# Optimization experiments

Hardware: AMD Instinct MI355X
Metric: run time of the kernel (lower is better)

The kernel has to match this reference:

```python
import jax, jax.numpy as jnp
import numpy as np

N_HEAD = 16
N_EMBD = 1024


def setup_inputs() -> dict:
    key = jax.random.key(0)
    k1, k2 = jax.random.split(key)
    x = jax.random.normal(k1, (2, 2048, N_EMBD), dtype=jnp.float32)
    # nn.Linear(n_embd, 3*n_embd, bias=False); store as [in, out] for x @ w
    w_qkv = jax.random.normal(k2, (N_EMBD, 3 * N_EMBD), dtype=jnp.float32) * (N_EMBD ** -0.5)
    return {"x": x, "w_qkv": w_qkv}


def reference(x, w_qkv):
    B, T, C = x.shape
    H = N_HEAD
    D = C // H  # head dim
    qkv = x @ w_qkv  # [B, T, 3C]
    q, k, v = jnp.split(qkv, 3, axis=2)
    # [B, T, H, D] -> [B, H, T, D]
    q = q.reshape(B, T, H, D).transpose(0, 2, 1, 3)
    k = k.reshape(B, T, H, D).transpose(0, 2, 1, 3)
    v = v.reshape(B, T, H, D).transpose(0, 2, 1, 3)
    att = jnp.einsum('bhtd,bhsd->bhts', q, k) / np.sqrt(D).astype(np.float32)
    causal = jnp.tril(jnp.ones((T, T), dtype=bool))  # [T, T]
    att = jnp.where(causal, att, -jnp.inf)
    att = jax.nn.softmax(att, axis=-1)
    out = jnp.einsum('bhts,bhsd->bhtd', att, v)  # [B, H, T, D]
    return out.transpose(0, 2, 1, 3).reshape(B, T, C)
```

## Files before the change

kernel.cpp:

```cpp
#include <hip/hip_runtime.h>
#include <hip/hip_bf16.h>

#define BATCH 2
#define SEQ   2048
#define EMBD  1024
#define NHEAD 16
#define HDIM  64
#define N3    3072
#define MTOT  4096
#define KDIM  1024

typedef __attribute__((ext_vector_type(8))) short  short8;
typedef __attribute__((ext_vector_type(4))) short  s16x4;
typedef __attribute__((ext_vector_type(4))) unsigned short u16x4;
typedef __attribute__((ext_vector_type(4))) float  f32x4;

__device__ __forceinline__ unsigned short f2bf(float f) {
    unsigned int u = __builtin_bit_cast(unsigned int, f);
    u += 0x7fffu + ((u >> 16) & 1u);
    return (unsigned short)(u >> 16);
}

__global__ __launch_bounds__(256) void cast_x_kernel(const float* __restrict__ x,
                                                     short* __restrict__ xb, int n4) {
    int i = blockIdx.x * 256 + threadIdx.x;
    if (i >= n4) return;
    float4 f = reinterpret_cast<const float4*>(x)[i];
    s16x4 o;
    o[0] = (short)f2bf(f.x); o[1] = (short)f2bf(f.y);
    o[2] = (short)f2bf(f.z); o[3] = (short)f2bf(f.w);
    reinterpret_cast<s16x4*>(xb)[i] = o;
}

__global__ __launch_bounds__(256) void cast_wt_kernel(const float* __restrict__ w,
                                                      short* __restrict__ wt) {
    __shared__ float tile[32][33];
    int n0 = blockIdx.x * 32;
    int k0 = blockIdx.y * 32;
    int tx = threadIdx.x & 31;
    int ty = threadIdx.x >> 5;
#pragma unroll
    for (int i = 0; i < 4; ++i)
        tile[ty + i * 8][tx] = w[(size_t)(k0 + ty + i * 8) * N3 + n0 + tx];
    __syncthreads();
#pragma unroll
    for (int i = 0; i < 4; ++i)
        wt[(size_t)(n0 + ty + i * 8) * KDIM + k0 + tx] = (short)f2bf(tile[tx][ty + i * 8]);
}

__device__ __forceinline__ void stage_tile(const short* gbase, short* lbase, int tid) {
#pragma unroll
    for (int c = 0; c < 2; ++c) {
        int row = c * 64 + (tid >> 2);
        int chunk = tid & 3;
        const short* gp = gbase + (size_t)row * KDIM + chunk * 8;
        short* lp = lbase + c * 2048 + tid * 8;
        __builtin_amdgcn_global_load_lds((const __attribute__((address_space(1))) void*)gp,
                                         (__attribute__((address_space(3))) void*)lp,
                                         16, 0, 0);
    }
}

__global__ __launch_bounds__(256) void qkv_gemm_kernel(const short* __restrict__ xb,
                                                       const short* __restrict__ wt,
                                                       short* __restrict__ qb,
                                                       short* __restrict__ kbuf,
                                                       short* __restrict__ vt) {
    __shared__ short lA[2][128 * 32];
    __shared__ short lB[2][128 * 32];

    const int tid  = threadIdx.x;
    const int lane = tid & 63;
    const int wid  = tid >> 6;
    const int wm = wid >> 1, wn = wid & 1;
    const int m0 = blockIdx.y * 128;
    const int n0 = blockIdx.x * 128;

    f32x4 acc[4][4];
#pragma unroll
    for (int i = 0; i < 4; ++i)
#pragma unroll
        for (int j = 0; j < 4; ++j) acc[i][j] = (f32x4){0.f, 0.f, 0.f, 0.f};

    const short* gA = xb + (size_t)m0 * KDIM;
    const short* gB = wt + (size_t)n0 * KDIM;

    stage_tile(gA, lA[0], tid);
    stage_tile(gB, lB[0], tid);
    asm volatile("s_waitcnt vmcnt(0)" ::: "memory");
    __syncthreads();

    int cur = 0;
    const int arow = (lane & 15) * 32 + (lane >> 4) * 8;
#pragma unroll 1
    for (int kt = 0; kt < KDIM / 32; ++kt) {
        if (kt + 1 < KDIM / 32) {
            stage_tile(gA + (kt + 1) * 32, lA[cur ^ 1], tid);
            stage_tile(gB + (kt + 1) * 32, lB[cur ^ 1], tid);
        }
        short8 a[4], b[4];
#pragma unroll
        for (int im = 0; im < 4; ++im)
            a[im] = *(const short8*)&lA[cur][(wm * 64 + im * 16) * 32 + arow];
#pragma unroll
        for (int in = 0; in < 4; ++in)
            b[in] = *(const short8*)&lB[cur][(wn * 64 + in * 16) * 32 + arow];
#pragma unroll
        for (int im = 0; im < 4; ++im)
#pragma unroll
            for (int in = 0; in < 4; ++in)
                acc[im][in] = __builtin_amdgcn_mfma_f32_16x16x32_bf16(a[im], b[in], acc[im][in], 0, 0, 0);
        asm volatile("s_waitcnt vmcnt(0)" ::: "memory");
        __syncthreads();
        cur ^= 1;
    }

#pragma unroll
    for (int im = 0; im < 4; ++im) {
        int t0m = m0 + wm * 64 + im * 16 + (lane >> 4) * 4;
        int b = t0m >> 11;
        int t0 = t0m & 2047;
#pragma unroll
        for (int in = 0; in < 4; ++in) {
            int col = n0 + wn * 64 + in * 16 + (lane & 15);
            int which = col >> 10;
            int h = (col >> 6) & 15;
            int d = col & 63;
            if (which == 2) {
                u16x4 pk;
#pragma unroll
                for (int r = 0; r < 4; ++r) pk[r] = f2bf(acc[im][in][r]);
                *(u16x4*)&vt[((size_t)(b * NHEAD + h) * HDIM + d) * SEQ + t0] = pk;
            } else {
                short* dst = (which == 0) ? qb : kbuf;
#pragma unroll
                for (int r = 0; r < 4; ++r)
                    dst[((size_t)(b * NHEAD + h) * SEQ + t0 + r) * HDIM + d] = (short)f2bf(acc[im][in][r]);
            }
        }
    }
}

#define KVB 64

__device__ __forceinline__ int swzf(int r) { return (r & 3) ^ (((r >> 2) & 3) << 1); }

__device__ __forceinline__ void stage_kv(const short* kh, const short* vh, int kb,
                                         short* lk, short* lv, int tid) {
#pragma unroll
    for (int c = 0; c < 2; ++c) {
        int row = c * 32 + (tid >> 3);
        int sch = (tid & 7) ^ swzf(row);
        const short* gk = kh + (size_t)(kb + row) * HDIM + sch * 8;
        short* lpk = lk + c * 2048 + tid * 8;
        __builtin_amdgcn_global_load_lds((const __attribute__((address_space(1))) void*)gk,
                                         (__attribute__((address_space(3))) void*)lpk, 16, 0, 0);
        const short* gv = vh + (size_t)row * SEQ + kb + sch * 8;
        short* lpv = lv + c * 2048 + tid * 8;
        __builtin_amdgcn_global_load_lds((const __attribute__((address_space(1))) void*)gv,
                                         (__attribute__((address_space(3))) void*)lpv, 16, 0, 0);
    }
}

__global__ __launch_bounds__(256) void attn_kernel(const short* __restrict__ q,
                                                   const short* __restrict__ kk,
                                                   const short* __restrict__ vtg,
                                                   float* __restrict__ out) {
    const int tid  = threadIdx.x;
    const int lane = tid & 63;
    const int wid  = tid >> 6;
    const int pid = blockIdx.x;
    const int bh = blockIdx.y;
    const int rbase = lane & 15;
    const int hi    = lane >> 4;

    const short* qh = q   + (size_t)bh * SEQ * HDIM;
    const short* kh = kk  + (size_t)bh * SEQ * HDIM;
    const short* vh = vtg + (size_t)bh * HDIM * SEQ;

    __shared__ short lK[2][KVB * 64];
    __shared__ short lV[2][KVB * 64];

    const float L2E = 1.4426950408889634f;
    const float C1  = 0.125f * 1.4426950408889634f;
    short8 vone;
#pragma unroll
    for (int j = 0; j < 8; ++j) vone[j] = (short)0x3F80;

    const int b = bh >> 4, h = bh & 15;

#pragma unroll 1
    for (int seg = 0; seg < 2; ++seg) {
        const int qt = seg ? pid : (31 - pid);
        const int qbase = qt * 64 + wid * 16;
        const int qrow  = qbase + rbase;

        short8 aQ[2];
#pragma unroll
        for (int c = 0; c < 2; ++c)
            aQ[c] = *(const short8*)&qh[(size_t)qrow * HDIM + c * 32 + hi * 8];

        f32x4 o[4];
#pragma unroll
        for (int i = 0; i < 4; ++i) o[i] = (f32x4){0.f, 0.f, 0.f, 0.f};
        float mrun = -INFINITY;
        float lrun = 0.f;

        const int ktiles = qt + 1;
        stage_kv(kh, vh, 0, lK[0], lV[0], tid);
        int cur = 0;
#pragma unroll 1
        for (int t = 0; t < ktiles; ++t) {
            const int kb = t * KVB;
            if (t + 1 < ktiles) {
                stage_kv(kh, vh, kb + KVB, lK[cur ^ 1], lV[cur ^ 1], tid);
                asm volatile("s_waitcnt vmcnt(4) lgkmcnt(0)" ::: "memory");
            } else {
                asm volatile("s_waitcnt vmcnt(0) lgkmcnt(0)" ::: "memory");
            }
            __builtin_amdgcn_s_barrier();
            __builtin_amdgcn_sched_barrier(0);

            if (kb < qbase + 16) {
                const short* lk = lK[cur];
                const short* lv = lV[cur];
                f32x4 s[4];
                __builtin_amdgcn_s_setprio(1);
#pragma unroll
                for (int nb = 0; nb < 4; ++nb) {
                    int kidx = (nb & 1) * 32 + (rbase >> 2) * 8 + (nb >> 1) * 4 + (rbase & 3);
                    f32x4 a = (f32x4){0.f, 0.f, 0.f, 0.f};
#pragma unroll
                    for (int c = 0; c < 2; ++c) {
                        int slot = (c * 4 + hi) ^ swzf(kidx);
                        short8 bK = *(const short8*)&lk[kidx * 64 + slot * 8];
                        a = __builtin_amdgcn_mfma_f32_16x16x32_bf16(bK, aQ[c], a, 0, 0, 0);
                    }
                    s[nb] = a;
                }
                __builtin_amdgcn_s_setprio(0);
                if (kb + KVB - 1 > qbase) {
#pragma unroll
                    for (int nb = 0; nb < 4; ++nb) {
                        int keyb = kb + (nb & 1) * 32 + hi * 8 + (nb >> 1) * 4;
#pragma unroll
                        for (int r = 0; r < 4; ++r)
                            if (keyb + r > qrow) s[nb][r] = -1e30f;
                    }
                }
                float pm = fmaxf(fmaxf(fmaxf(s[0][0], s[0][1]), fmaxf(s[0][2], s[0][3])),
                                 fmaxf(fmaxf(s[1][0], s[1][1]), fmaxf(s[1][2], s[1][3])));
                float pm2 = fmaxf(fmaxf(fmaxf(s[2][0], s[2][1]), fmaxf(s[2][2], s[2][3])),
                                  fmaxf(fmaxf(s[3][0], s[3][1]), fmaxf(s[3][2], s[3][3])));
                pm = fmaxf(pm, pm2);
                pm = fmaxf(pm, __shfl_xor(pm, 16));
                pm = fmaxf(pm, __shfl_xor(pm, 32));
                pm *= 0.125f;
                if (__any(pm > mrun)) {
                    float mnew = fmaxf(mrun, pm);
                    float sf = exp2f((mrun - mnew) * L2E);
                    mrun = mnew;
                    lrun *= sf;
#pragma unroll
                    for (int dt = 0; dt < 4; ++dt)
#pragma unroll
                        for (int r = 0; r < 4; ++r) o[dt][r] *= sf;
                }
                float mterm = mrun * L2E;
                short8 bp[2];
#pragma unroll
                for (int c = 0; c < 2; ++c)
#pragma unroll
                    for (int j = 0; j < 8; ++j) {
                        float p = exp2f(fmaf(s[c + (j >> 2) * 2][j & 3], C1, -mterm));
                        bp[c][j] = (short)f2bf(p);
                    }
                f32x4 osum = (f32x4){0.f, 0.f, 0.f, 0.f};
                __builtin_amdgcn_s_setprio(1);
#pragma unroll
                for (int dt = 0; dt < 4; ++dt) {
                    int d = dt * 16 + rbase;
#pragma unroll
                    for (int c = 0; c < 2; ++c) {
                        int slot = (c * 4 + hi) ^ swzf(d);
                        short8 bV = *(const short8*)&lv[d * 64 + slot * 8];
                        o[dt] = __builtin_amdgcn_mfma_f32_16x16x32_bf16(bV, bp[c], o[dt], 0, 0, 0);
                    }
                }
#pragma unroll
                for (int c = 0; c < 2; ++c)
                    osum = __builtin_amdgcn_mfma_f32_16x16x32_bf16(vone, bp[c], osum, 0, 0, 0);
                __builtin_amdgcn_s_setprio(0);
                lrun += osum[0];
            }
            __builtin_amdgcn_sched_barrier(0);
            __builtin_amdgcn_s_barrier();
            cur ^= 1;
        }

        float inv = 1.0f / lrun;
#pragma unroll
        for (int dt = 0; dt < 4; ++dt) {
            f32x4 ov;
#pragma unroll
            for (int r = 0; r < 4; ++r) ov[r] = o[dt][r] * inv;
            *(f32x4*)&out[((size_t)(b * SEQ + qrow) * NHEAD + h) * HDIM + dt * 16 + hi * 4] = ov;
        }
    }
}

extern "C" void kernel_launch(void* const* d_in, const int* in_sizes, int n_in,
                              void* d_out, int out_size, void* d_ws, size_t ws_size,
                              hipStream_t stream) {
    const float* x = (const float*)d_in[0];
    const float* w = (const float*)d_in[1];
    float* out = (float*)d_out;

    char* ws = (char*)d_ws;
    short* xb   = (short*)(ws);
    short* wt   = (short*)(ws + (size_t)8  * 1024 * 1024);
    short* qb   = (short*)(ws + (size_t)14 * 1024 * 1024);
    short* kbuf = (short*)(ws + (size_t)22 * 1024 * 1024);
    short* vt   = (short*)(ws + (size_t)30 * 1024 * 1024);

    cast_x_kernel<<<dim3(MTOT * KDIM / 4 / 256), dim3(256), 0, stream>>>(x, xb, MTOT * KDIM / 4);
    cast_wt_kernel<<<dim3(N3 / 32, KDIM / 32), dim3(256), 0, stream>>>(w, wt);
    qkv_gemm_kernel<<<dim3(N3 / 128, MTOT / 128), dim3(256), 0, stream>>>(xb, wt, qb, kbuf, vt);
    attn_kernel<<<dim3(16, BATCH * NHEAD), dim3(256), 0, stream>>>(qb, kbuf, vt, out);
}
```

Before: 109.0 us.

## Use intrinsic bf16 conversion, XCD-aware attention grid, and lazy max rescaling

```diff
diff --git a/kernel.cpp b/kernel.cpp
--- a/kernel.cpp
+++ b/kernel.cpp
@@ -12,13 +12,10 @@
 
 typedef __attribute__((ext_vector_type(8))) short  short8;
 typedef __attribute__((ext_vector_type(4))) short  s16x4;
-typedef __attribute__((ext_vector_type(4))) unsigned short u16x4;
 typedef __attribute__((ext_vector_type(4))) float  f32x4;
 
-__device__ __forceinline__ unsigned short f2bf(float f) {
-    unsigned int u = __builtin_bit_cast(unsigned int, f);
-    u += 0x7fffu + ((u >> 16) & 1u);
-    return (unsigned short)(u >> 16);
+__device__ __forceinline__ short f2bfs(float f) {
+    return __builtin_bit_cast(short, __float2bfloat16(f));
 }
 
 __global__ __launch_bounds__(256) void cast_x_kernel(const float* __restrict__ x,
@@ -27,8 +24,8 @@
     if (i >= n4) return;
     float4 f = reinterpret_cast<const float4*>(x)[i];
     s16x4 o;
-    o[0] = (short)f2bf(f.x); o[1] = (short)f2bf(f.y);
-    o[2] = (short)f2bf(f.z); o[3] = (short)f2bf(f.w);
+    o[0] = f2bfs(f.x); o[1] = f2bfs(f.y);
+    o[2] = f2bfs(f.z); o[3] = f2bfs(f.w);
     reinterpret_cast<s16x4*>(xb)[i] = o;
 }
 
@@ -45,7 +42,7 @@
     __syncthreads();
 #pragma unroll
     for (int i = 0; i < 4; ++i)
-        wt[(size_t)(n0 + ty + i * 8) * KDIM + k0 + tx] = (short)f2bf(tile[tx][ty + i * 8]);
+        wt[(size_t)(n0 + ty + i * 8) * KDIM + k0 + tx] = f2bfs(tile[tx][ty + i * 8]);
 }
 
 __device__ __forceinline__ void stage_tile(const short* gbase, short* lbase, int tid) {
@@ -127,15 +124,15 @@
             int h = (col >> 6) & 15;
             int d = col & 63;
             if (which == 2) {
-                u16x4 pk;
-#pragma unroll
-                for (int r = 0; r < 4; ++r) pk[r] = f2bf(acc[im][in][r]);
-                *(u16x4*)&vt[((size_t)(b * NHEAD + h) * HDIM + d) * SEQ + t0] = pk;
+                s16x4 pk;
+#pragma unroll
+                for (int r = 0; r < 4; ++r) pk[r] = f2bfs(acc[im][in][r]);
+                *(s16x4*)&vt[((size_t)(b * NHEAD + h) * HDIM + d) * SEQ + t0] = pk;
             } else {
                 short* dst = (which == 0) ? qb : kbuf;
 #pragma unroll
                 for (int r = 0; r < 4; ++r)
-                    dst[((size_t)(b * NHEAD + h) * SEQ + t0 + r) * HDIM + d] = (short)f2bf(acc[im][in][r]);
+                    dst[((size_t)(b * NHEAD + h) * SEQ + t0 + r) * HDIM + d] = f2bfs(acc[im][in][r]);
             }
         }
     }
@@ -169,8 +166,11 @@
     const int tid  = threadIdx.x;
     const int lane = tid & 63;
     const int wid  = tid >> 6;
-    const int pid = blockIdx.x;
-    const int bh = blockIdx.y;
+    const int lid  = blockIdx.x;
+    const int xcd  = lid & 7;
+    const int rest = lid >> 3;
+    const int pid  = rest & 15;
+    const int bh   = (rest >> 4) * 8 + xcd;
     const int rbase = lane & 15;
     const int hi    = lane >> 4;
 
@@ -256,7 +256,7 @@
                 pm = fmaxf(pm, __shfl_xor(pm, 16));
                 pm = fmaxf(pm, __shfl_xor(pm, 32));
                 pm *= 0.125f;
-                if (__any(pm > mrun)) {
+                if (__any(pm > mrun + 8.0f)) {
                     float mnew = fmaxf(mrun, pm);
                     float sf = exp2f((mrun - mnew) * L2E);
                     mrun = mnew;
@@ -273,7 +273,7 @@
 #pragma unroll
                     for (int j = 0; j < 8; ++j) {
                         float p = exp2f(fmaf(s[c + (j >> 2) * 2][j & 3], C1, -mterm));
-                        bp[c][j] = (short)f2bf(p);
+                        bp[c][j] = f2bfs(p);
                     }
                 f32x4 osum = (f32x4){0.f, 0.f, 0.f, 0.f};
                 __builtin_amdgcn_s_setprio(1);
@@ -326,5 +326,5 @@
     cast_x_kernel<<<dim3(MTOT * KDIM / 4 / 256), dim3(256), 0, stream>>>(x, xb, MTOT * KDIM / 4);
     cast_wt_kernel<<<dim3(N3 / 32, KDIM / 32), dim3(256), 0, stream>>>(w, wt);
     qkv_gemm_kernel<<<dim3(N3 / 128, MTOT / 128), dim3(256), 0, stream>>>(xb, wt, qb, kbuf, vt);
-    attn_kernel<<<dim3(16, BATCH * NHEAD), dim3(256), 0, stream>>>(qb, kbuf, vt, out);
-}
+    attn_kernel<<<dim3(512), dim3(256), 0, stream>>>(qb, kbuf, vt, out);
+}
```

After: 101.7 us. -6.7%, faster.
